# Performance work log

Measured on AMD Instinct MI355X. Metric: run time of the kernel, lower is better.

The kernel has to match this reference:

```python
import jax, jax.numpy as jnp
import numpy as np

H = 1024
W = 1024
K = 3  # kernel_size
N = H * W
TWO_PI = 2.0 * np.pi


def setup_inputs() -> dict:
    key = jax.random.key(0)
    ks = jax.random.split(key, 8)
    latent = jax.random.normal(ks[0], (H, W, 4), dtype=jnp.float32)
    raw_pos = jax.random.randint(ks[1], (N, 2), 0, W, dtype=jnp.int32)
    control = jax.random.normal(ks[2], (N, 2), dtype=jnp.float32)
    def lin(k, fan_in, fan_out):
        bound = 1.0 / np.sqrt(fan_in)
        return jax.random.uniform(k, (fan_in, fan_out), jnp.float32, -bound, bound)
    W1 = lin(ks[3], 108, 64); b1 = jnp.zeros((64,), jnp.float32)
    W2 = lin(ks[4], 64, 128); b2 = jnp.zeros((128,), jnp.float32)
    W3 = lin(ks[5], 128, 64); b3 = jnp.zeros((64,), jnp.float32)
    W4 = lin(ks[6], 64, 4);   b4 = jnp.zeros((4,), jnp.float32)
    return dict(latent=latent, raw_pos=raw_pos, control=control,
                W1=W1, b1=b1, W2=W2, b2=b2, W3=W3, b3=b3, W4=W4, b4=b4)


def reference(latent, raw_pos, control, W1, b1, W2, b2, W3, b3, W4, b4):
    # --- kernel expand: 3x3 neighbor coords, clamped at edges ---
    offs = jnp.arange(-(K // 2), K // 2 + 1)
    xo, yo = jnp.meshgrid(offs, offs, indexing='ij')  # [K,K]
    ex = jnp.clip(raw_pos[:, 0:1] + xo.ravel()[None, :], 0, W - 1)  # [N, K*K]
    ey = jnp.clip(raw_pos[:, 1:2] + yo.ravel()[None, :], 0, H - 1)  # [N, K*K]

    # --- neighbor gather via computed linear indices ---
    lin_idx = ey * W + ex                                   # [N, K*K]
    latent_values = latent.reshape(-1, latent.shape[-1])[lin_idx]  # [N, K*K, 4]

    # --- positional encodings (num_encodings=6, non-exponential) ---
    xf = ex.astype(jnp.float32) / W                         # already clamped
    yf = ey.astype(jnp.float32) / H
    pos_enc = jnp.stack([
        xf, yf,
        jnp.sin(TWO_PI * 1 * xf), jnp.sin(TWO_PI * 1 * yf),
        jnp.sin(TWO_PI * 2 * xf), jnp.sin(TWO_PI * 2 * yf),
    ], axis=-1)                                             # [N, K*K, 6]

    # --- control broadcast across kernel positions ---
    ctrl = jnp.broadcast_to(control[:, None, :], (control.shape[0], K * K, control.shape[-1]))

    patches = jnp.concatenate([latent_values, pos_enc, ctrl], axis=-1)  # [N, K*K, 12]
    x = patches.reshape(patches.shape[0], -1)               # [N, 108]

    # --- tiny MLP: Linear+GELU(exact) x3, Linear+Sigmoid ---
    gelu = lambda t: jax.nn.gelu(t, approximate=False)
    x = gelu(x @ W1 + b1)
    x = gelu(x @ W2 + b2)
    x = gelu(x @ W3 + b3)
    return jax.nn.sigmoid(x @ W4 + b4)                      # [N, 4]
```

## Files before the change

kernel.cpp:

```cpp
#include <hip/hip_runtime.h>
#include <hip/hip_bf16.h>
#include <math.h>

#define IMG 1024
#define NPIXTOT (IMG * IMG)
#define TWO_PI_F 6.28318530717958647692f

typedef __attribute__((ext_vector_type(8))) short short8;
typedef __attribute__((ext_vector_type(4))) float f32x4;
typedef unsigned int uint;
typedef unsigned short ushort;

#define A1_OFF 0
#define A2_OFF 8192
#define A3_OFF 16384
#define A4_OFF 24576
#define WTOT   25600
#define GLUT_N   3072
#define GLUT_OFF WTOT
#define SLUT_OFF (GLUT_OFF + GLUT_N)
#define SLUT_N   2048
#define WSTOT    (SLUT_OFF + SLUT_N)

#define LATBF_BYTEOFF 65536

__device__ __forceinline__ ushort f2bf(float f) {
    uint u = __float_as_uint(f);
    u += 0x7fffu + ((u >> 16) & 1u);
    return (ushort)(u >> 16);
}
__device__ __forceinline__ uint pack2(float a, float b) {
    float2 t; t.x = a; t.y = b;
    __hip_bfloat162 h = __float22bfloat162_rn(t);
    union { __hip_bfloat162 h; uint u; } cv; cv.h = h;
    return cv.u;
}
__device__ __forceinline__ float sig_fast(float x) {
    return __builtin_amdgcn_rcpf(1.0f + __expf(-x));
}

__device__ __forceinline__ uint gelu2(float x0, float x1, const ushort* g) {
    union { uint u; ushort h[2]; } w;
    w.h[0] = g[(int)__builtin_amdgcn_fmed3f(fmaf(x0, 256.0f, 1536.5f), 0.0f, 3071.0f)];
    w.h[1] = g[(int)__builtin_amdgcn_fmed3f(fmaf(x1, 256.0f, 1536.5f), 0.0f, 3071.0f)];
    return w.u;
}

__device__ __forceinline__ int permM(int k) {
    return (2 * (k >> 5) + ((k >> 2) & 1)) * 16 + 4 * ((k >> 3) & 3) + (k & 3);
}

__device__ __forceinline__ int2 nbc(int2 rp, int n) {
    const int dxi = (n * 86) >> 8;
    int2 c;
    c.x = min(max(rp.x + dxi - 1, 0), IMG - 1);
    c.y = min(max(rp.y + (n - 3 * dxi) - 1, 0), IMG - 1);
    return c;
}

__global__ void prep_weights(const float* __restrict__ W1, const float* __restrict__ b1,
                             const float* __restrict__ W2, const float* __restrict__ W3,
                             const float* __restrict__ W4, ushort* __restrict__ ws) {
    int e = blockIdx.x * 256 + threadIdx.x;
    if (e >= WSTOT) return;
    float v;
    if (e < A2_OFF) {
        int i = e & 7, lo = (e >> 3) & 15, hi = (e >> 7) & 3, kst = e >> 9;
        int ks = kst & 3;
        int m = (kst >> 2) * 16 + lo;
        int korig;
        if (ks < 2)       korig = 12 * (2 * hi + ks) + i;
        else if (ks == 2) korig = 12 * (2 * hi + (i >> 2)) + 8 + (i & 3);
        else {
            if (hi == 0)      korig = 96 + i;
            else if (hi == 1) korig = (i < 4) ? 104 + i : (i == 4 ? 108 : 999);
            else              korig = 999;
        }
        v = (korig < 108) ? W1[korig * 64 + m] : (korig == 108 ? b1[m] : 0.0f);
    } else if (e < A3_OFF) {
        int r = e - A2_OFF, i = r & 7, lo = (r >> 3) & 15, hi = (r >> 7) & 3, kst = r >> 9;
        int m = (kst >> 1) * 16 + lo, k = (kst & 1) * 32 + hi * 8 + i;
        v = W2[permM(k) * 128 + m];
    } else if (e < A4_OFF) {
        int r = e - A3_OFF, i = r & 7, lo = (r >> 3) & 15, hi = (r >> 7) & 3, kst = r >> 9;
        int m = (kst >> 2) * 16 + lo, k = (kst & 3) * 32 + hi * 8 + i;
        v = W3[permM(k) * 64 + m];
    } else if (e < GLUT_OFF) {
        int r = e - A4_OFF, i = r & 7, lo = (r >> 3) & 15, hi = (r >> 7) & 3, ks = (r >> 9) & 1;
        int k = ks * 32 + hi * 8 + i;
        v = (lo < 4) ? W4[permM(k) * 4 + lo] : 0.0f;
    } else if (e < SLUT_OFF) {
        const float x = (float)(e - GLUT_OFF - 1536) * (1.0f / 256.0f);
        v = 0.5f * x * (1.0f + erff(x * 0.70710678118654752440f));
    } else {
        const int j = e - SLUT_OFF;
        const float a = (float)(j >> 1) * (1.0f / 1024.0f);
        v = sinf(((j & 1) ? 2.0f : 1.0f) * TWO_PI_F * a);
    }
    ws[e] = f2bf(v);
}

__global__ void prep_latent(const float* __restrict__ lat, ushort* __restrict__ dst) {
    const int i = blockIdx.x * 256 + threadIdx.x;
    if (i >= NPIXTOT) return;
    const float4 v = ((const float4*)lat)[i];
    union { ushort h[4]; uint2 u; } o;
    o.h[0] = f2bf(v.x); o.h[1] = f2bf(v.y); o.h[2] = f2bf(v.z); o.h[3] = f2bf(v.w);
    ((uint2*)dst)[i] = o.u;
}

template<int KS, int KSN, bool HASB>
__device__ __forceinline__ void mlayer_pf(const short8 (&bin)[2][KS], short8 (&bout)[2][KSN],
                                          const ushort* wA,
                                          const float* __restrict__ bias,
                                          const ushort* gl, int lo, int hi) {
    const int lane8 = (hi * 16 + lo) * 8;
    short8 a[2][2 * KS];
    #pragma unroll
    for (int t = 0; t < 2 * KS; ++t)
        a[0][t] = *(const short8*)&wA[t * 512 + lane8];

    #pragma unroll
    for (int kn = 0; kn < KSN; ++kn) {
        if (kn + 1 < KSN) {
            #pragma unroll
            for (int t = 0; t < 2 * KS; ++t)
                a[(kn + 1) & 1][t] =
                    *(const short8*)&wA[((kn + 1) * 2 * KS + t) * 512 + lane8];
        }
        f32x4 acc[2][2];
        #pragma unroll
        for (int b = 0; b < 2; ++b) {
            if (HASB) {
                const float4 bv = *(const float4*)&bias[(2 * kn + b) * 16 + hi * 4];
                acc[b][0] = f32x4{bv.x, bv.y, bv.z, bv.w};
            } else {
                acc[b][0] = f32x4{0.f, 0.f, 0.f, 0.f};
            }
            acc[b][1] = acc[b][0];
            #pragma unroll
            for (int ks = 0; ks < KS; ++ks) {
                const short8 av = a[kn & 1][b * KS + ks];
                acc[b][0] = __builtin_amdgcn_mfma_f32_16x16x32_bf16(av, bin[0][ks], acc[b][0], 0, 0, 0);
                acc[b][1] = __builtin_amdgcn_mfma_f32_16x16x32_bf16(av, bin[1][ks], acc[b][1], 0, 0, 0);
            }
        }
        #pragma unroll
        for (int pt = 0; pt < 2; ++pt) {
            union { short8 s; uint u[4]; } o;
            o.u[0] = gelu2(acc[0][pt][0], acc[0][pt][1], gl);
            o.u[1] = gelu2(acc[0][pt][2], acc[0][pt][3], gl);
            o.u[2] = gelu2(acc[1][pt][0], acc[1][pt][1], gl);
            o.u[3] = gelu2(acc[1][pt][2], acc[1][pt][3], gl);
            bout[pt][kn] = o.s;
        }
    }
}

template<bool BF>
__global__ __launch_bounds__(512, 4) void vfx_mfma(
    const float* __restrict__ latent, const uint2* __restrict__ latbf,
    const int* __restrict__ raw_pos, const float* __restrict__ control,
    const ushort* __restrict__ wsrc,
    const float* __restrict__ b2, const float* __restrict__ b3,
    const float* __restrict__ b4, float* __restrict__ out)
{
    __shared__ ushort wl[WSTOT];
    const int tid = threadIdx.x;
    const int wave = tid >> 6, lane = tid & 63;
    const int lo = lane & 15, hi = lane >> 4;
    const int pixbase = blockIdx.x * 256 + wave * 32;

    {
        const uint4* src = (const uint4*)wsrc;
        uint4* dst = (uint4*)wl;
        #pragma unroll
        for (int it = 0; it < 8; ++it) {
            const int i = tid + it * 512;
            if (i < 3840) dst[i] = src[i];
        }
    }

    const int g0 = pixbase + lo, g1 = pixbase + 16 + lo;
    const int2 rp0 = ((const int2*)raw_pos)[g0];
    const int2 rp1 = ((const int2*)raw_pos)[g1];
    const float2 cf0 = ((const float2*)control)[g0];
    const float2 cf1 = ((const float2*)control)[g1];

    const int na = 2 * hi, nbb = 2 * hi + 1;
    const int2 cA0 = nbc(rp0, na), cB0 = nbc(rp0, nbb);
    const int2 cA1 = nbc(rp1, na), cB1 = nbc(rp1, nbb);
    const int2 c80 = nbc(rp0, 8),  c81 = nbc(rp1, 8);

    uint2 lA0, lB0, lA1, lB1, l80, l81;
    if (BF) {
        lA0 = latbf[(cA0.y << 10) + cA0.x]; lB0 = latbf[(cB0.y << 10) + cB0.x];
        lA1 = latbf[(cA1.y << 10) + cA1.x]; lB1 = latbf[(cB1.y << 10) + cB1.x];
        if (hi == 0) { l80 = latbf[(c80.y << 10) + c80.x]; l81 = latbf[(c81.y << 10) + c81.x]; }
    } else {
        const float4* lf = (const float4*)latent;
        float4 a;
        a = lf[(cA0.y << 10) + cA0.x]; lA0 = make_uint2(pack2(a.x, a.y), pack2(a.z, a.w));
        a = lf[(cB0.y << 10) + cB0.x]; lB0 = make_uint2(pack2(a.x, a.y), pack2(a.z, a.w));
        a = lf[(cA1.y << 10) + cA1.x]; lA1 = make_uint2(pack2(a.x, a.y), pack2(a.z, a.w));
        a = lf[(cB1.y << 10) + cB1.x]; lB1 = make_uint2(pack2(a.x, a.y), pack2(a.z, a.w));
        if (hi == 0) {
            a = lf[(c80.y << 10) + c80.x]; l80 = make_uint2(pack2(a.x, a.y), pack2(a.z, a.w));
            a = lf[(c81.y << 10) + c81.x]; l81 = make_uint2(pack2(a.x, a.y), pack2(a.z, a.w));
        }
    }

    __syncthreads();
    const ushort* glut = wl + GLUT_OFF;
    const uint*   slut = (const uint*)(wl + SLUT_OFF);

    short8 bX[2][4];
    {
        auto mk = [&](int2 c, uint2 lat, uint& s2u) -> short8 {
            const uint sx = slut[c.x], sy = slut[c.y];
            s2u = (sx >> 16) | (sy & 0xffff0000u);
            union { short8 s; uint u[4]; } o;
            o.u[0] = lat.x; o.u[1] = lat.y;
            o.u[2] = pack2((float)c.x * (1.0f / IMG), (float)c.y * (1.0f / IMG));
            o.u[3] = (sx & 0xffffu) | (sy << 16);
            return o.s;
        };
        uint s2a0, s2b0, s2a1, s2b1;
        bX[0][0] = mk(cA0, lA0, s2a0);
        bX[0][1] = mk(cB0, lB0, s2b0);
        bX[1][0] = mk(cA1, lA1, s2a1);
        bX[1][1] = mk(cB1, lB1, s2b1);
        const uint upc0 = pack2(cf0.x, cf0.y), upc1 = pack2(cf1.x, cf1.y);
        union { short8 s; uint u[4]; } t;
        t.u[0] = s2a0; t.u[1] = upc0; t.u[2] = s2b0; t.u[3] = upc0; bX[0][2] = t.s;
        t.u[0] = s2a1; t.u[1] = upc1; t.u[2] = s2b1; t.u[3] = upc1; bX[1][2] = t.s;
        if (hi == 0) {
            uint d0, d1;
            bX[0][3] = mk(c80, l80, d0);
            bX[1][3] = mk(c81, l81, d1);
        } else if (hi == 1) {
            union { short8 s; uint u[4]; } o;
            o.u[0] = (slut[c80.x] >> 16) | (slut[c80.y] & 0xffff0000u);
            o.u[1] = upc0; o.u[2] = 0x3f80u; o.u[3] = 0u;
            bX[0][3] = o.s;
            o.u[0] = (slut[c81.x] >> 16) | (slut[c81.y] & 0xffff0000u);
            o.u[1] = upc1;
            bX[1][3] = o.s;
        } else {
            union { short8 s; uint u[4]; } z;
            z.u[0] = 0u; z.u[1] = 0u; z.u[2] = 0u; z.u[3] = 0u;
            bX[0][3] = z.s; bX[1][3] = z.s;
        }
    }

    short8 h1[2][2], h2[2][4], h3[2][2];
    mlayer_pf<4, 2, false>(bX, h1, wl + A1_OFF, nullptr, glut, lo, hi);
    mlayer_pf<2, 4, true >(h1, h2, wl + A2_OFF, b2, glut, lo, hi);
    mlayer_pf<4, 2, true >(h2, h3, wl + A3_OFF, b3, glut, lo, hi);

    {
        float4 bv = {0.f, 0.f, 0.f, 0.f};
        if (hi == 0) bv = *(const float4*)b4;
        f32x4 acc0 = {bv.x, bv.y, bv.z, bv.w};
        f32x4 acc1 = acc0;
        #pragma unroll
        for (int ks = 0; ks < 2; ++ks) {
            const short8 a = *(const short8*)&wl[A4_OFF + (ks * 512) + (hi * 16 + lo) * 8];
            acc0 = __builtin_amdgcn_mfma_f32_16x16x32_bf16(a, h3[0][ks], acc0, 0, 0, 0);
            acc1 = __builtin_amdgcn_mfma_f32_16x16x32_bf16(a, h3[1][ks], acc1, 0, 0, 0);
        }
        if (hi == 0) {
            float4 o;
            o.x = sig_fast(acc0[0]); o.y = sig_fast(acc0[1]);
            o.z = sig_fast(acc0[2]); o.w = sig_fast(acc0[3]);
            *(float4*)&out[(pixbase + lo) * 4] = o;
            o.x = sig_fast(acc1[0]); o.y = sig_fast(acc1[1]);
            o.z = sig_fast(acc1[2]); o.w = sig_fast(acc1[3]);
            *(float4*)&out[(pixbase + 16 + lo) * 4] = o;
        }
    }
}

extern "C" void kernel_launch(void* const* d_in, const int* in_sizes, int n_in,
                              void* d_out, int out_size, void* d_ws, size_t ws_size,
                              hipStream_t stream) {
    const float* latent  = (const float*)d_in[0];
    const int*   raw_pos = (const int*)  d_in[1];
    const float* control = (const float*)d_in[2];
    const float* W1 = (const float*)d_in[3];
    const float* b1 = (const float*)d_in[4];
    const float* W2 = (const float*)d_in[5];
    const float* b2 = (const float*)d_in[6];
    const float* W3 = (const float*)d_in[7];
    const float* b3 = (const float*)d_in[8];
    const float* W4 = (const float*)d_in[9];
    const float* b4 = (const float*)d_in[10];
    float* out = (float*)d_out;
    ushort* ws = (ushort*)d_ws;

    prep_weights<<<dim3((WSTOT + 255) / 256), dim3(256), 0, stream>>>(W1, b1, W2, W3, W4, ws);

    const size_t need = (size_t)LATBF_BYTEOFF + (size_t)NPIXTOT * 8;
    const bool use_bf = ws_size >= need;
    dim3 grid(NPIXTOT / 256);

    if (use_bf) {
        ushort* latbf = (ushort*)((char*)d_ws + LATBF_BYTEOFF);
        prep_latent<<<dim3(NPIXTOT / 256), dim3(256), 0, stream>>>(latent, latbf);
        vfx_mfma<true><<<grid, dim3(512), 0, stream>>>(
            latent, (const uint2*)latbf, raw_pos, control, ws, b2, b3, b4, out);
    } else {
        vfx_mfma<false><<<grid, dim3(512), 0, stream>>>(
            latent, nullptr, raw_pos, control, ws, b2, b3, b4, out);
    }
}
```

Measured before the change: 101.2 us.

## Compact LDS tables, compute sin in hardware, raise occupancy hint

Removes the sine lookup table and computes positional sin terms with hardware sin on fractional turns. Shrinks the GELU LUT range and stores only the four useful rows of the last-layer weights, cutting LDS size and the staging copy. Raises the launch-bounds minimum blocks per CU from 4 to 6 to allow more concurrency. This risks register spills and adds transcendental ALU work in exchange for less LDS and fewer LDS lookups.

```diff
diff --git a/kernel.cpp b/kernel.cpp
--- a/kernel.cpp
+++ b/kernel.cpp
@@ -14,13 +14,10 @@
 #define A1_OFF 0
 #define A2_OFF 8192
 #define A3_OFF 16384
-#define A4_OFF 24576
-#define WTOT   25600
-#define GLUT_N   3072
-#define GLUT_OFF WTOT
-#define SLUT_OFF (GLUT_OFF + GLUT_N)
-#define SLUT_N   2048
-#define WSTOT    (SLUT_OFF + SLUT_N)
+#define A4C_OFF 24576
+#define GLUT_OFF 24832
+#define GLUT_N   2304
+#define WSTOT    27136
 
 #define LATBF_BYTEOFF 65536
 
@@ -41,8 +38,8 @@
 
 __device__ __forceinline__ uint gelu2(float x0, float x1, const ushort* g) {
     union { uint u; ushort h[2]; } w;
-    w.h[0] = g[(int)__builtin_amdgcn_fmed3f(fmaf(x0, 256.0f, 1536.5f), 0.0f, 3071.0f)];
-    w.h[1] = g[(int)__builtin_amdgcn_fmed3f(fmaf(x1, 256.0f, 1536.5f), 0.0f, 3071.0f)];
+    w.h[0] = g[(int)__builtin_amdgcn_fmed3f(fmaf(x0, 256.0f, 1024.5f), 0.0f, 2303.0f)];
+    w.h[1] = g[(int)__builtin_amdgcn_fmed3f(fmaf(x1, 256.0f, 1024.5f), 0.0f, 2303.0f)];
     return w.u;
 }
 
@@ -81,21 +78,17 @@
         int r = e - A2_OFF, i = r & 7, lo = (r >> 3) & 15, hi = (r >> 7) & 3, kst = r >> 9;
         int m = (kst >> 1) * 16 + lo, k = (kst & 1) * 32 + hi * 8 + i;
         v = W2[permM(k) * 128 + m];
-    } else if (e < A4_OFF) {
+    } else if (e < A4C_OFF) {
         int r = e - A3_OFF, i = r & 7, lo = (r >> 3) & 15, hi = (r >> 7) & 3, kst = r >> 9;
         int m = (kst >> 2) * 16 + lo, k = (kst & 3) * 32 + hi * 8 + i;
         v = W3[permM(k) * 64 + m];
     } else if (e < GLUT_OFF) {
-        int r = e - A4_OFF, i = r & 7, lo = (r >> 3) & 15, hi = (r >> 7) & 3, ks = (r >> 9) & 1;
+        int r = e - A4C_OFF, i = r & 7, l4 = (r >> 3) & 3, hi = (r >> 5) & 3, ks = (r >> 7) & 1;
         int k = ks * 32 + hi * 8 + i;
-        v = (lo < 4) ? W4[permM(k) * 4 + lo] : 0.0f;
-    } else if (e < SLUT_OFF) {
-        const float x = (float)(e - GLUT_OFF - 1536) * (1.0f / 256.0f);
+        v = W4[permM(k) * 4 + l4];
+    } else {
+        const float x = (float)(e - GLUT_OFF - 1024) * (1.0f / 256.0f);
         v = 0.5f * x * (1.0f + erff(x * 0.70710678118654752440f));
-    } else {
-        const int j = e - SLUT_OFF;
-        const float a = (float)(j >> 1) * (1.0f / 1024.0f);
-        v = sinf(((j & 1) ? 2.0f : 1.0f) * TWO_PI_F * a);
     }
     ws[e] = f2bf(v);
 }
@@ -158,7 +151,7 @@
 }
 
 template<bool BF>
-__global__ __launch_bounds__(512, 4) void vfx_mfma(
+__global__ __launch_bounds__(512, 6) void vfx_mfma(
     const float* __restrict__ latent, const uint2* __restrict__ latbf,
     const int* __restrict__ raw_pos, const float* __restrict__ control,
     const ushort* __restrict__ wsrc,
@@ -175,9 +168,9 @@
         const uint4* src = (const uint4*)wsrc;
         uint4* dst = (uint4*)wl;
         #pragma unroll
-        for (int it = 0; it < 8; ++it) {
+        for (int it = 0; it < 7; ++it) {
             const int i = tid + it * 512;
-            if (i < 3840) dst[i] = src[i];
+            if (i < WSTOT / 8) dst[i] = src[i];
         }
     }
 
@@ -212,17 +205,20 @@
 
     __syncthreads();
     const ushort* glut = wl + GLUT_OFF;
-    const uint*   slut = (const uint*)(wl + SLUT_OFF);
 
     short8 bX[2][4];
     {
         auto mk = [&](int2 c, uint2 lat, uint& s2u) -> short8 {
-            const uint sx = slut[c.x], sy = slut[c.y];
-            s2u = (sx >> 16) | (sy & 0xffff0000u);
+            const float xf = (float)c.x * (1.0f / IMG), yf = (float)c.y * (1.0f / IMG);
+            const float s1x = __builtin_amdgcn_sinf(xf);
+            const float s1y = __builtin_amdgcn_sinf(yf);
+            const float s2x = __builtin_amdgcn_sinf(__builtin_amdgcn_fractf(2.0f * xf));
+            const float s2y = __builtin_amdgcn_sinf(__builtin_amdgcn_fractf(2.0f * yf));
+            s2u = pack2(s2x, s2y);
             union { short8 s; uint u[4]; } o;
             o.u[0] = lat.x; o.u[1] = lat.y;
-            o.u[2] = pack2((float)c.x * (1.0f / IMG), (float)c.y * (1.0f / IMG));
-            o.u[3] = (sx & 0xffffu) | (sy << 16);
+            o.u[2] = pack2(xf, yf);
+            o.u[3] = pack2(s1x, s1y);
             return o.s;
         };
         uint s2a0, s2b0, s2a1, s2b1;
@@ -240,10 +236,14 @@
             bX[1][3] = mk(c81, l81, d1);
         } else if (hi == 1) {
             union { short8 s; uint u[4]; } o;
-            o.u[0] = (slut[c80.x] >> 16) | (slut[c80.y] & 0xffff0000u);
+            o.u[0] = pack2(
+                __builtin_amdgcn_sinf(__builtin_amdgcn_fractf(2.0f * (float)c80.x * (1.0f / IMG))),
+                __builtin_amdgcn_sinf(__builtin_amdgcn_fractf(2.0f * (float)c80.y * (1.0f / IMG))));
             o.u[1] = upc0; o.u[2] = 0x3f80u; o.u[3] = 0u;
             bX[0][3] = o.s;
-            o.u[0] = (slut[c81.x] >> 16) | (slut[c81.y] & 0xffff0000u);
+            o.u[0] = pack2(
+                __builtin_amdgcn_sinf(__builtin_amdgcn_fractf(2.0f * (float)c81.x * (1.0f / IMG))),
+                __builtin_amdgcn_sinf(__builtin_amdgcn_fractf(2.0f * (float)c81.y * (1.0f / IMG))));
             o.u[1] = upc1;
             bX[1][3] = o.s;
         } else {
@@ -265,7 +265,7 @@
         f32x4 acc1 = acc0;
         #pragma unroll
         for (int ks = 0; ks < 2; ++ks) {
-            const short8 a = *(const short8*)&wl[A4_OFF + (ks * 512) + (hi * 16 + lo) * 8];
+            const short8 a = *(const short8*)&wl[A4C_OFF + ks * 128 + (hi * 4 + (lo & 3)) * 8];
             acc0 = __builtin_amdgcn_mfma_f32_16x16x32_bf16(a, h3[0][ks], acc0, 0, 0, 0);
             acc1 = __builtin_amdgcn_mfma_f32_16x16x32_bf16(a, h3[1][ks], acc1, 0, 0, 0);
         }
```

Result: slower. 164.2 us (+62.3%).
